# Kernel optimization log

Hardware: AMD Instinct MI355X
Metric: run time of the kernel (lower is better)

The kernel has to match this reference:

```python
import jax, jax.numpy as jnp
import numpy as np
from jax import lax

B, S, N, DIM = 4, 512, 16, 8
D_MODEL, D_STATE = 1024, 64
INPUT_SIZE = N * DIM
LN_EPS = 1e-5


def setup_inputs() -> dict:
    key = jax.random.key(0)
    ks = jax.random.split(key, 8)
    s = 0.02
    x = jax.random.normal(ks[0], (B, S, N, DIM), dtype=jnp.float32)
    W_emb = jax.random.normal(ks[1], (INPUT_SIZE, D_MODEL), dtype=jnp.float32) * s
    b_emb = jnp.zeros((D_MODEL,), jnp.float32)
    W_xp = jax.random.normal(ks[2], (D_MODEL, 2 * D_STATE + 1), dtype=jnp.float32) * s
    b_xp = jnp.zeros((2 * D_STATE + 1,), jnp.float32)
    # A init: -exp(arange(1, d_state+1) * 0.1), matching the torch module
    A = -jnp.exp(jnp.arange(1, D_STATE + 1, dtype=jnp.float32) * 0.1)
    Dp = jnp.ones((D_MODEL,), jnp.float32)
    gamma = jnp.ones((D_MODEL,), jnp.float32)
    beta = jnp.zeros((D_MODEL,), jnp.float32)
    W_out = jax.random.normal(ks[3], (D_MODEL, INPUT_SIZE), dtype=jnp.float32) * s
    b_out = jnp.zeros((INPUT_SIZE,), jnp.float32)
    return {"x": x, "W_emb": W_emb, "b_emb": b_emb, "W_xp": W_xp, "b_xp": b_xp,
            "A": A, "Dp": Dp, "gamma": gamma, "beta": beta,
            "W_out": W_out, "b_out": b_out}


def reference(x, W_emb, b_emb, W_xp, b_xp, A, Dp, gamma, beta, W_out, b_out):
    b, s, n, dim = x.shape
    d_state = A.shape[0]
    d_model = W_emb.shape[1]
    u = x.reshape(b, s, n * dim) @ W_emb + b_emb            # [B,S,dm]
    sel = u @ W_xp + b_xp                                    # [B,S,2*ds+1]
    delta = jax.nn.softplus(sel[..., 0:1]) * 0.01            # [B,S,1]
    Bs = sel[..., 1:1 + d_state]                             # [B,S,ds]
    Cs = sel[..., 1 + d_state:]                              # [B,S,ds]
    A_bar = jnp.exp(delta * A)                               # [B,S,ds]
    B_bar = delta * Bs                                       # [B,S,ds]

    def step(h, inp):
        a_t, b_t, c_t, u_t = inp                             # [B,ds],[B,ds],[B,ds],[B,dm]
        h = h * a_t[:, None, :] + b_t[:, None, :] * u_t[:, :, None]  # [B,dm,ds]
        y_t = jnp.einsum('bmd,bd->bm', h, c_t) + u_t * Dp
        return h, y_t

    h0 = jnp.zeros((b, d_model, d_state), x.dtype)
    xs = (jnp.swapaxes(A_bar, 0, 1), jnp.swapaxes(B_bar, 0, 1),
          jnp.swapaxes(Cs, 0, 1), jnp.swapaxes(u, 0, 1))
    _, ys = lax.scan(step, h0, xs)                           # ys: [S,B,dm]
    y = jnp.swapaxes(ys, 0, 1)                               # [B,S,dm]
    mu = y.mean(-1, keepdims=True)
    var = y.var(-1, keepdims=True)
    yn = (y - mu) / jnp.sqrt(var + LN_EPS) * gamma + beta
    pred = yn @ W_out + b_out                                # [B,S,N*D]
    return pred.reshape(b, s, n, dim)
```

## Files before the change

### kernel.cpp

```cpp
#include <hip/hip_runtime.h>
#include <cstddef>

typedef __attribute__((ext_vector_type(8))) short short8;
typedef __attribute__((ext_vector_type(4))) float f32x4;

constexpr int ROWS = 2048;
constexpr int CL   = 32;

__device__ inline ushort tobf(float f) {
  union { float f; unsigned u; } v; v.f = f;
  return (ushort)((v.u + 0x7FFFu + ((v.u >> 16) & 1u)) >> 16);
}

__global__ __launch_bounds__(256)
void prep(const float* __restrict__ Wemb, const float* __restrict__ Wxp,
          const float* __restrict__ Wout, const float* __restrict__ x,
          ushort* __restrict__ WembT, ushort* __restrict__ wBCdT,
          ushort* __restrict__ WoutT, ushort* __restrict__ xbf) {
  int idx = blockIdx.x * 256 + threadIdx.x;
  if (idx < 131072) {
    int n = idx >> 7, k = idx & 127;
    WembT[idx] = tobf(Wemb[k * 1024 + n]);
  } else if (idx < 327680) {
    int j = idx - 131072;
    int n = j >> 10, k = j & 1023;
    float v = (n < 128) ? Wxp[k * 129 + 1 + n] : (n == 128 ? Wxp[k * 129] : 0.f);
    wBCdT[j] = tobf(v);
  } else if (idx < 458752) {
    int j = idx - 327680;
    int n = j >> 10, k = j & 1023;
    WoutT[j] = tobf(Wout[k * 128 + n]);
  } else if (idx < 720896) {
    int j = idx - 458752;
    xbf[j] = tobf(x[j]);
  }
}

template<bool SPLIT>
__global__ __launch_bounds__(256)
void gemm_bt_bf16(const ushort* __restrict__ A, const ushort* __restrict__ BT,
                  const float* __restrict__ bias, float* __restrict__ C,
                  ushort* __restrict__ Cbf, int M, int N, int K) {
  __shared__ __align__(16) ushort sA[8192];
  __shared__ __align__(16) ushort sB[8192];
  const int t  = threadIdx.x;
  const int n0 = blockIdx.x * 64;
  const int m0 = blockIdx.y * 64;
  const int kc = blockIdx.z << 7;

  #pragma unroll
  for (int i = 0; i < 4; ++i) {
    int c = t + (i << 8);
    int row = c >> 4, kk = (c & 15) << 3;
    float4 va = *(const float4*)(A  + (size_t)(m0 + row) * K + kc + kk);
    float4 vb = *(const float4*)(BT + (size_t)(n0 + row) * K + kc + kk);
    int byteoff = ((row << 8) + (kk << 1)) ^ ((row & 7) << 4);
    *(float4*)((char*)sA + byteoff) = va;
    *(float4*)((char*)sB + byteoff) = vb;
  }
  __syncthreads();

  const int lane = t & 63, w = t >> 6;
  const int wr = w << 4;
  const int colsel = lane & 15;
  const int kg = lane >> 4;

  short8 a[4];
  {
    int arow = wr + colsel;
    int lin = (arow << 8) + (kg << 4);
    int swz = (arow & 7) << 4;
    #pragma unroll
    for (int ks = 0; ks < 4; ++ks)
      a[ks] = *(const short8*)((const char*)sA + ((lin + (ks << 6)) ^ swz));
  }

  f32x4 acc[4];
  #pragma unroll
  for (int nf = 0; nf < 4; ++nf) acc[nf] = (f32x4)(0.f);

  #pragma unroll
  for (int nf = 0; nf < 4; ++nf) {
    int brow = (nf << 4) + colsel;
    int lin = (brow << 8) + (kg << 4);
    int swz = (brow & 7) << 4;
    #pragma unroll
    for (int ks = 0; ks < 4; ++ks) {
      short8 b = *(const short8*)((const char*)sB + ((lin + (ks << 6)) ^ swz));
      acc[nf] = __builtin_amdgcn_mfma_f32_16x16x32_bf16(a[ks], b, acc[nf], 0, 0, 0);
    }
  }

  const int r4 = kg << 2;
  float* Cp = C;
  if (SPLIT) Cp += (size_t)blockIdx.z * (size_t)M * N;
  #pragma unroll
  for (int nf = 0; nf < 4; ++nf) {
    int gn = n0 + (nf << 4) + colsel;
    #pragma unroll
    for (int reg = 0; reg < 4; ++reg) {
      int gm = m0 + wr + r4 + reg;
      if (SPLIT) {
        Cp[(size_t)gm * N + gn] = acc[nf][reg];
      } else {
        float v = acc[nf][reg] + bias[gn];
        C[(size_t)gm * N + gn] = v;
        Cbf[(size_t)gm * N + gn] = tobf(v);
      }
    }
  }
}

__global__ __launch_bounds__(256)
void k2e_epilogue(const float* __restrict__ part, const float* __restrict__ bxp,
                  const float* __restrict__ A, float* __restrict__ abc) {
  int gid = blockIdx.x * 256 + threadIdx.x;
  int row = gid >> 6, d = gid & 63;
  const size_t PN = (size_t)ROWS * 192;
  float sb = 0.f, sc = 0.f, dr = 0.f;
  #pragma unroll
  for (int z = 0; z < 8; ++z) {
    const float* p = part + z * PN + (size_t)row * 192;
    sb += p[d];
    sc += p[64 + d];
    dr += p[128];
  }
  sb += bxp[1 + d];
  sc += bxp[65 + d];
  float xv = dr + bxp[0];
  float sp = (xv > 15.f) ? xv : log1pf(__expf(xv));
  float delta = 0.01f * sp;
  float* o = abc + (size_t)row * 192;
  o[d]       = __expf(delta * A[d]);
  o[64 + d]  = delta * sb;
  o[128 + d] = sc;
}

__global__ __launch_bounds__(256)
void scan_sum(const float* __restrict__ u, const float* __restrict__ abc,
              float* __restrict__ cst, float* __restrict__ Ach) {
  __shared__ __align__(16) float sbuf[CL * 192];
  const int t = threadIdx.x, lane = t & 63, w = t >> 6;
  const int tc = blockIdx.x % 15;
  const int mg = (blockIdx.x / 15) & 3;
  const int b  = blockIdx.x / 60;
  const int r0 = b * 512 + tc * CL;

  const float4* src = (const float4*)(abc + (size_t)r0 * 192);
  #pragma unroll
  for (int i = 0; i < 6; ++i)
    ((float4*)sbuf)[t + i * 256] = src[t + i * 256];
  __syncthreads();

  const int m = (mg * 4 + w) * 64 + lane;
  const float* ub = u + (size_t)r0 * 1024 + m;
  const bool doAp = (mg == 0 && w == 0);

  float2 h[32];
  float2 ap[32];
  #pragma unroll
  for (int j = 0; j < 32; ++j) { h[j] = make_float2(0.f, 0.f); ap[j] = make_float2(1.f, 1.f); }

  float u0 = ub[0];
  float u1 = ub[1024];
  for (int s = 0; s < CL; ++s) {
    int sn = (s < CL - 3) ? s + 2 : CL - 1;
    float u2 = ub[(size_t)sn * 1024];
    const float* L = sbuf + s * 192;
    #pragma unroll
    for (int jj = 0; jj < 16; ++jj) {
      float4 a4 = *(const float4*)&L[4 * jj];
      float4 b4 = *(const float4*)&L[64 + 4 * jj];
      h[2 * jj].x     = fmaf(h[2 * jj].x,     a4.x, b4.x * u0);
      h[2 * jj].y     = fmaf(h[2 * jj].y,     a4.y, b4.y * u0);
      h[2 * jj + 1].x = fmaf(h[2 * jj + 1].x, a4.z, b4.z * u0);
      h[2 * jj + 1].y = fmaf(h[2 * jj + 1].y, a4.w, b4.w * u0);
    }
    if (doAp) {
      #pragma unroll
      for (int jj = 0; jj < 16; ++jj) {
        float4 a4 = *(const float4*)&L[4 * jj];
        ap[2 * jj].x     *= a4.x;
        ap[2 * jj].y     *= a4.y;
        ap[2 * jj + 1].x *= a4.z;
        ap[2 * jj + 1].y *= a4.w;
      }
    }
    u0 = u1; u1 = u2;
  }

  size_t cbase = (((size_t)b * 15 + tc) * 64) * 1024 + m;
  #pragma unroll
  for (int j = 0; j < 32; ++j) {
    cst[cbase + (size_t)(2 * j)     * 1024] = h[j].x;
    cst[cbase + (size_t)(2 * j + 1) * 1024] = h[j].y;
  }
  if (doAp && lane == 0) {
    float2* ad = (float2*)&Ach[((size_t)b * 15 + tc) * 64];
    #pragma unroll
    for (int j = 0; j < 32; ++j) ad[j] = ap[j];
  }
}

__global__ __launch_bounds__(256)
void scan_comb(float* __restrict__ cst, const float* __restrict__ Ach) {
  int g = blockIdx.x * 256 + threadIdx.x;
  int b = g >> 16;
  int rem = g & 65535;
  int d = rem >> 10;
  int m = rem & 1023;
  float h = 0.f;
  for (int t2 = 0; t2 < 15; ++t2) {
    size_t idx = (((size_t)(b * 15 + t2)) * 64 + d) * 1024 + m;
    h = fmaf(Ach[(b * 15 + t2) * 64 + d], h, cst[idx]);
    cst[idx] = h;
  }
}

__global__ __launch_bounds__(256)
void scan_out(const float* __restrict__ u, const float* __restrict__ abc,
              const float* __restrict__ cst, const float* __restrict__ Dp,
              float* __restrict__ y) {
  __shared__ __align__(16) float sbuf[CL * 192];
  const int t = threadIdx.x, lane = t & 63, w = t >> 6;
  const int tc = blockIdx.x & 15;
  const int mg = (blockIdx.x >> 4) & 3;
  const int b  = blockIdx.x >> 6;
  const int r0 = b * 512 + tc * CL;

  const float4* src = (const float4*)(abc + (size_t)r0 * 192);
  #pragma unroll
  for (int i = 0; i < 6; ++i)
    ((float4*)sbuf)[t + i * 256] = src[t + i * 256];
  __syncthreads();

  const int m = (mg * 4 + w) * 64 + lane;
  const float* ub = u + (size_t)r0 * 1024 + m;
  float*       yb = y + (size_t)r0 * 1024 + m;
  const float dp = Dp[m];

  float2 h[32];
  if (tc == 0) {
    #pragma unroll
    for (int j = 0; j < 32; ++j) h[j] = make_float2(0.f, 0.f);
  } else {
    size_t cbase = (((size_t)b * 15 + (tc - 1)) * 64) * 1024 + m;
    #pragma unroll
    for (int j = 0; j < 32; ++j) {
      h[j].x = cst[cbase + (size_t)(2 * j)     * 1024];
      h[j].y = cst[cbase + (size_t)(2 * j + 1) * 1024];
    }
  }

  float u0 = ub[0];
  float u1 = ub[1024];
  for (int s = 0; s < CL; ++s) {
    int sn = (s < CL - 3) ? s + 2 : CL - 1;
    float u2 = ub[(size_t)sn * 1024];
    const float* L = sbuf + s * 192;
    float y0 = 0.f, y1 = 0.f, y2 = 0.f, y3 = 0.f;
    #pragma unroll
    for (int jj = 0; jj < 16; ++jj) {
      float4 a4 = *(const float4*)&L[4 * jj];
      float4 b4 = *(const float4*)&L[64 + 4 * jj];
      float4 c4 = *(const float4*)&L[128 + 4 * jj];
      h[2 * jj].x     = fmaf(h[2 * jj].x,     a4.x, b4.x * u0);
      h[2 * jj].y     = fmaf(h[2 * jj].y,     a4.y, b4.y * u0);
      h[2 * jj + 1].x = fmaf(h[2 * jj + 1].x, a4.z, b4.z * u0);
      h[2 * jj + 1].y = fmaf(h[2 * jj + 1].y, a4.w, b4.w * u0);
      y0 = fmaf(c4.x, h[2 * jj].x,     y0);
      y1 = fmaf(c4.y, h[2 * jj].y,     y1);
      y2 = fmaf(c4.z, h[2 * jj + 1].x, y2);
      y3 = fmaf(c4.w, h[2 * jj + 1].y, y3);
    }
    yb[(size_t)s * 1024] = (y0 + y1) + (y2 + y3) + u0 * dp;
    u0 = u1; u1 = u2;
  }
}

__global__ __launch_bounds__(256)
void k4a_ln(const float* __restrict__ y, const float* __restrict__ gamma,
            const float* __restrict__ beta, ushort* __restrict__ ynbf) {
  __shared__ float red[8];
  int t = threadIdx.x, lane = t & 63, wv = t >> 6;
  int row = blockIdx.x;
  float4 v = *(const float4*)&y[(size_t)row * 1024 + t * 4];
  float s1 = v.x + v.y + v.z + v.w;
  float s2 = v.x * v.x + v.y * v.y + v.z * v.z + v.w * v.w;
  #pragma unroll
  for (int o = 32; o; o >>= 1) {
    s1 += __shfl_xor(s1, o, 64);
    s2 += __shfl_xor(s2, o, 64);
  }
  if (lane == 0) { red[wv] = s1; red[4 + wv] = s2; }
  __syncthreads();
  float S1 = red[0] + red[1] + red[2] + red[3];
  float S2 = red[4] + red[5] + red[6] + red[7];
  float mean = S1 * (1.f / 1024.f);
  float var  = S2 * (1.f / 1024.f) - mean * mean;
  float rstd = rsqrtf(var + 1e-5f);
  float4 g  = *(const float4*)&gamma[t * 4];
  float4 be = *(const float4*)&beta[t * 4];
  ushort4 o;
  o.x = tobf((v.x - mean) * rstd * g.x + be.x);
  o.y = tobf((v.y - mean) * rstd * g.y + be.y);
  o.z = tobf((v.z - mean) * rstd * g.z + be.z);
  o.w = tobf((v.w - mean) * rstd * g.w + be.w);
  *(ushort4*)&ynbf[(size_t)row * 1024 + t * 4] = o;
}

__global__ __launch_bounds__(256)
void k4c_out(const float* __restrict__ part, const float* __restrict__ bout,
             float* __restrict__ out) {
  int g4 = blockIdx.x * 256 + threadIdx.x;
  size_t idx = (size_t)g4 * 4;
  const size_t PN = (size_t)ROWS * 128;
  float4 s = *(const float4*)&part[idx];
  #pragma unroll
  for (int z = 1; z < 8; ++z) {
    float4 p = *(const float4*)&part[z * PN + idx];
    s.x += p.x; s.y += p.y; s.z += p.z; s.w += p.w;
  }
  float4 bb = *(const float4*)&bout[idx & 127];
  s.x += bb.x; s.y += bb.y; s.z += bb.z; s.w += bb.w;
  *(float4*)&out[idx] = s;
}

extern "C" void kernel_launch(void* const* d_in, const int* in_sizes, int n_in,
                              void* d_out, int out_size, void* d_ws, size_t ws_size,
                              hipStream_t stream) {
  const float* x     = (const float*)d_in[0];
  const float* W_emb = (const float*)d_in[1];
  const float* b_emb = (const float*)d_in[2];
  const float* W_xp  = (const float*)d_in[3];
  const float* b_xp  = (const float*)d_in[4];
  const float* A     = (const float*)d_in[5];
  const float* Dp    = (const float*)d_in[6];
  const float* gamma = (const float*)d_in[7];
  const float* beta  = (const float*)d_in[8];
  const float* W_out = (const float*)d_in[9];
  const float* b_out = (const float*)d_in[10];
  float* out = (float*)d_out;
  float* ws  = (float*)d_ws;

  float* u    = ws;
  float* y    = u + 2097152;
  float* abc  = y + 2097152;
  float* part = abc + 393216;
  float* cst  = part + 3145728;
  float* Ach  = cst + 3932160;
  ushort* ubf   = (ushort*)(Ach + 4096);
  ushort* ynbf  = ubf + 2097152;
  ushort* xbf   = ynbf + 2097152;
  ushort* WembT = xbf + 262144;
  ushort* wBCdT = WembT + 131072;
  ushort* WoutT = wBCdT + 196608;

  prep<<<2816, 256, 0, stream>>>(W_emb, W_xp, W_out, x, WembT, wBCdT, WoutT, xbf);
  gemm_bt_bf16<false><<<dim3(16, 32, 1), 256, 0, stream>>>(
      xbf, WembT, b_emb, u, ubf, 2048, 1024, 128);
  gemm_bt_bf16<true><<<dim3(3, 32, 8), 256, 0, stream>>>(
      ubf, wBCdT, nullptr, part, nullptr, 2048, 192, 1024);
  k2e_epilogue<<<512, 256, 0, stream>>>(part, b_xp, A, abc);
  scan_sum<<<240, 256, 0, stream>>>(u, abc, cst, Ach);
  scan_comb<<<1024, 256, 0, stream>>>(cst, Ach);
  scan_out<<<256, 256, 0, stream>>>(u, abc, cst, Dp, y);
  k4a_ln<<<2048, 256, 0, stream>>>(y, gamma, beta, ynbf);
  gemm_bt_bf16<true><<<dim3(2, 32, 8), 256, 0, stream>>>(
      ynbf, WoutT, nullptr, part, nullptr, 2048, 128, 1024);
  k4c_out<<<256, 256, 0, stream>>>(part, b_out, out);
}
```

Baseline: 156.6 us.

## Fuse all stages into one persistent kernel with grid-wide barriers

Replaces the ten-launch pipeline with a single persistent 256-block kernel that runs each stage in sequence, separated by atomic-counter grid barriers. Split-K partial buffers and their reduction kernels are dropped in favour of atomicAdd into pre-initialised outputs, and the scans read the bf16 copy of u instead of an fp32 copy. The aim is to remove launch overhead and the extra partial-sum traffic. In exchange, the spin barriers require all 256 blocks to be co-resident, fewer blocks are available for the larger phases, and atomic accumulation makes the summation order nondeterministic.

```diff
diff --git a/kernel.cpp b/kernel.cpp
--- a/kernel.cpp
+++ b/kernel.cpp
@@ -4,369 +4,371 @@
 typedef __attribute__((ext_vector_type(8))) short short8;
 typedef __attribute__((ext_vector_type(4))) float f32x4;
 
-constexpr int ROWS = 2048;
-constexpr int CL   = 32;
+constexpr int CL = 32;
+constexpr int NB = 256;
 
 __device__ inline ushort tobf(float f) {
   union { float f; unsigned u; } v; v.f = f;
   return (ushort)((v.u + 0x7FFFu + ((v.u >> 16) & 1u)) >> 16);
 }
-
-__global__ __launch_bounds__(256)
-void prep(const float* __restrict__ Wemb, const float* __restrict__ Wxp,
-          const float* __restrict__ Wout, const float* __restrict__ x,
-          ushort* __restrict__ WembT, ushort* __restrict__ wBCdT,
-          ushort* __restrict__ WoutT, ushort* __restrict__ xbf) {
-  int idx = blockIdx.x * 256 + threadIdx.x;
-  if (idx < 131072) {
-    int n = idx >> 7, k = idx & 127;
-    WembT[idx] = tobf(Wemb[k * 1024 + n]);
-  } else if (idx < 327680) {
-    int j = idx - 131072;
-    int n = j >> 10, k = j & 1023;
-    float v = (n < 128) ? Wxp[k * 129 + 1 + n] : (n == 128 ? Wxp[k * 129] : 0.f);
-    wBCdT[j] = tobf(v);
-  } else if (idx < 458752) {
-    int j = idx - 327680;
-    int n = j >> 10, k = j & 1023;
-    WoutT[j] = tobf(Wout[k * 128 + n]);
-  } else if (idx < 720896) {
-    int j = idx - 458752;
-    xbf[j] = tobf(x[j]);
-  }
-}
-
-template<bool SPLIT>
-__global__ __launch_bounds__(256)
-void gemm_bt_bf16(const ushort* __restrict__ A, const ushort* __restrict__ BT,
-                  const float* __restrict__ bias, float* __restrict__ C,
-                  ushort* __restrict__ Cbf, int M, int N, int K) {
-  __shared__ __align__(16) ushort sA[8192];
-  __shared__ __align__(16) ushort sB[8192];
-  const int t  = threadIdx.x;
-  const int n0 = blockIdx.x * 64;
-  const int m0 = blockIdx.y * 64;
-  const int kc = blockIdx.z << 7;
-
-  #pragma unroll
-  for (int i = 0; i < 4; ++i) {
-    int c = t + (i << 8);
-    int row = c >> 4, kk = (c & 15) << 3;
-    float4 va = *(const float4*)(A  + (size_t)(m0 + row) * K + kc + kk);
-    float4 vb = *(const float4*)(BT + (size_t)(n0 + row) * K + kc + kk);
-    int byteoff = ((row << 8) + (kk << 1)) ^ ((row & 7) << 4);
-    *(float4*)((char*)sA + byteoff) = va;
-    *(float4*)((char*)sB + byteoff) = vb;
-  }
+__device__ inline float frombf(ushort u) {
+  union { unsigned u; float f; } v; v.u = ((unsigned)u) << 16; return v.f;
+}
+
+__global__ void bar_init(unsigned* cnt) {
+  if (threadIdx.x < 16) cnt[threadIdx.x] = 0;
+}
+
+__device__ __forceinline__ void gbar(unsigned* cnt, int phase) {
   __syncthreads();
+  if (threadIdx.x == 0) {
+    __threadfence();
+    atomicAdd(&cnt[phase], 1u);
+    while (__hip_atomic_load(&cnt[phase], __ATOMIC_RELAXED,
+                             __HIP_MEMORY_SCOPE_AGENT) < (unsigned)NB)
+      __builtin_amdgcn_s_sleep(2);
+    __threadfence();
+  }
+  __syncthreads();
+}
+
+template<int MODE>
+__device__ __forceinline__ void gemm_phase(
+    int vb, int nxt, int kchunk,
+    const ushort* __restrict__ Ab, const ushort* __restrict__ BT,
+    const float* __restrict__ bias, float* __restrict__ Cf,
+    ushort* __restrict__ Cbf, int M, int N, int K, char* SMEM) {
+  ushort* sA = (ushort*)SMEM;
+  ushort* sB = (ushort*)(SMEM + 16384);
+  const int t = threadIdx.x;
+  const int bx = vb % nxt;
+  const int rest = vb / nxt;
+  const int by = rest & 31;
+  const int bz = rest >> 5;
+  const int n0 = bx * 64, m0 = by * 64;
+  const int k0 = (MODE == 1) ? bz * kchunk : 0;
+  const int k1 = (MODE == 1) ? k0 + kchunk : K;
 
   const int lane = t & 63, w = t >> 6;
   const int wr = w << 4;
   const int colsel = lane & 15;
   const int kg = lane >> 4;
 
-  short8 a[4];
-  {
-    int arow = wr + colsel;
-    int lin = (arow << 8) + (kg << 4);
-    int swz = (arow & 7) << 4;
-    #pragma unroll
-    for (int ks = 0; ks < 4; ++ks)
-      a[ks] = *(const short8*)((const char*)sA + ((lin + (ks << 6)) ^ swz));
-  }
-
   f32x4 acc[4];
   #pragma unroll
   for (int nf = 0; nf < 4; ++nf) acc[nf] = (f32x4)(0.f);
 
-  #pragma unroll
-  for (int nf = 0; nf < 4; ++nf) {
-    int brow = (nf << 4) + colsel;
-    int lin = (brow << 8) + (kg << 4);
-    int swz = (brow & 7) << 4;
-    #pragma unroll
-    for (int ks = 0; ks < 4; ++ks) {
-      short8 b = *(const short8*)((const char*)sB + ((lin + (ks << 6)) ^ swz));
-      acc[nf] = __builtin_amdgcn_mfma_f32_16x16x32_bf16(a[ks], b, acc[nf], 0, 0, 0);
-    }
-  }
-
+  for (int kc = k0; kc < k1; kc += 128) {
+    __syncthreads();
+    #pragma unroll
+    for (int i = 0; i < 4; ++i) {
+      int c = t + (i << 8);
+      int row = c >> 4, kk = (c & 15) << 3;
+      float4 va  = *(const float4*)(Ab + (size_t)(m0 + row) * K + kc + kk);
+      float4 vb4 = *(const float4*)(BT + (size_t)(n0 + row) * K + kc + kk);
+      int byteoff = ((row << 8) + (kk << 1)) ^ ((row & 7) << 4);
+      *(float4*)((char*)sA + byteoff) = va;
+      *(float4*)((char*)sB + byteoff) = vb4;
+    }
+    __syncthreads();
+    short8 a[4];
+    {
+      int arow = wr + colsel;
+      int lin = (arow << 8) + (kg << 4);
+      int swz = (arow & 7) << 4;
+      #pragma unroll
+      for (int ks = 0; ks < 4; ++ks)
+        a[ks] = *(const short8*)((const char*)sA + ((lin + (ks << 6)) ^ swz));
+    }
+    #pragma unroll
+    for (int nf = 0; nf < 4; ++nf) {
+      int brow = (nf << 4) + colsel;
+      int lin = (brow << 8) + (kg << 4);
+      int swz = (brow & 7) << 4;
+      #pragma unroll
+      for (int ks = 0; ks < 4; ++ks) {
+        short8 b = *(const short8*)((const char*)sB + ((lin + (ks << 6)) ^ swz));
+        acc[nf] = __builtin_amdgcn_mfma_f32_16x16x32_bf16(a[ks], b, acc[nf], 0, 0, 0);
+      }
+    }
+  }
   const int r4 = kg << 2;
-  float* Cp = C;
-  if (SPLIT) Cp += (size_t)blockIdx.z * (size_t)M * N;
   #pragma unroll
   for (int nf = 0; nf < 4; ++nf) {
     int gn = n0 + (nf << 4) + colsel;
     #pragma unroll
     for (int reg = 0; reg < 4; ++reg) {
       int gm = m0 + wr + r4 + reg;
-      if (SPLIT) {
-        Cp[(size_t)gm * N + gn] = acc[nf][reg];
+      if (MODE == 0) {
+        Cbf[(size_t)gm * N + gn] = tobf(acc[nf][reg] + bias[gn]);
       } else {
-        float v = acc[nf][reg] + bias[gn];
-        C[(size_t)gm * N + gn] = v;
-        Cbf[(size_t)gm * N + gn] = tobf(v);
-      }
-    }
-  }
-}
-
-__global__ __launch_bounds__(256)
-void k2e_epilogue(const float* __restrict__ part, const float* __restrict__ bxp,
-                  const float* __restrict__ A, float* __restrict__ abc) {
-  int gid = blockIdx.x * 256 + threadIdx.x;
-  int row = gid >> 6, d = gid & 63;
-  const size_t PN = (size_t)ROWS * 192;
-  float sb = 0.f, sc = 0.f, dr = 0.f;
-  #pragma unroll
-  for (int z = 0; z < 8; ++z) {
-    const float* p = part + z * PN + (size_t)row * 192;
-    sb += p[d];
-    sc += p[64 + d];
-    dr += p[128];
-  }
-  sb += bxp[1 + d];
-  sc += bxp[65 + d];
-  float xv = dr + bxp[0];
-  float sp = (xv > 15.f) ? xv : log1pf(__expf(xv));
-  float delta = 0.01f * sp;
-  float* o = abc + (size_t)row * 192;
-  o[d]       = __expf(delta * A[d]);
-  o[64 + d]  = delta * sb;
-  o[128 + d] = sc;
-}
-
-__global__ __launch_bounds__(256)
-void scan_sum(const float* __restrict__ u, const float* __restrict__ abc,
-              float* __restrict__ cst, float* __restrict__ Ach) {
-  __shared__ __align__(16) float sbuf[CL * 192];
+        atomicAdd(&Cf[(size_t)gm * N + gn], acc[nf][reg]);
+      }
+    }
+  }
+}
+
+__global__ __launch_bounds__(256) void mamba_mega(
+    const float* __restrict__ x, const float* __restrict__ Wemb,
+    const float* __restrict__ bemb, const float* __restrict__ Wxp,
+    const float* __restrict__ bxp, const float* __restrict__ A,
+    const float* __restrict__ Dp, const float* __restrict__ gamma,
+    const float* __restrict__ beta, const float* __restrict__ Wout,
+    const float* __restrict__ bout, float* __restrict__ out,
+    float* __restrict__ ws) {
+  const int bid = blockIdx.x;
   const int t = threadIdx.x, lane = t & 63, w = t >> 6;
-  const int tc = blockIdx.x % 15;
-  const int mg = (blockIdx.x / 15) & 3;
-  const int b  = blockIdx.x / 60;
-  const int r0 = b * 512 + tc * CL;
-
-  const float4* src = (const float4*)(abc + (size_t)r0 * 192);
-  #pragma unroll
-  for (int i = 0; i < 6; ++i)
-    ((float4*)sbuf)[t + i * 256] = src[t + i * 256];
-  __syncthreads();
-
-  const int m = (mg * 4 + w) * 64 + lane;
-  const float* ub = u + (size_t)r0 * 1024 + m;
-  const bool doAp = (mg == 0 && w == 0);
-
-  float2 h[32];
-  float2 ap[32];
-  #pragma unroll
-  for (int j = 0; j < 32; ++j) { h[j] = make_float2(0.f, 0.f); ap[j] = make_float2(1.f, 1.f); }
-
-  float u0 = ub[0];
-  float u1 = ub[1024];
-  for (int s = 0; s < CL; ++s) {
-    int sn = (s < CL - 3) ? s + 2 : CL - 1;
-    float u2 = ub[(size_t)sn * 1024];
-    const float* L = sbuf + s * 192;
-    #pragma unroll
-    for (int jj = 0; jj < 16; ++jj) {
-      float4 a4 = *(const float4*)&L[4 * jj];
-      float4 b4 = *(const float4*)&L[64 + 4 * jj];
-      h[2 * jj].x     = fmaf(h[2 * jj].x,     a4.x, b4.x * u0);
-      h[2 * jj].y     = fmaf(h[2 * jj].y,     a4.y, b4.y * u0);
-      h[2 * jj + 1].x = fmaf(h[2 * jj + 1].x, a4.z, b4.z * u0);
-      h[2 * jj + 1].y = fmaf(h[2 * jj + 1].y, a4.w, b4.w * u0);
-    }
-    if (doAp) {
-      #pragma unroll
-      for (int jj = 0; jj < 16; ++jj) {
-        float4 a4 = *(const float4*)&L[4 * jj];
-        ap[2 * jj].x     *= a4.x;
-        ap[2 * jj].y     *= a4.y;
-        ap[2 * jj + 1].x *= a4.z;
-        ap[2 * jj + 1].y *= a4.w;
-      }
-    }
-    u0 = u1; u1 = u2;
-  }
-
-  size_t cbase = (((size_t)b * 15 + tc) * 64) * 1024 + m;
-  #pragma unroll
-  for (int j = 0; j < 32; ++j) {
-    cst[cbase + (size_t)(2 * j)     * 1024] = h[j].x;
-    cst[cbase + (size_t)(2 * j + 1) * 1024] = h[j].y;
-  }
-  if (doAp && lane == 0) {
-    float2* ad = (float2*)&Ach[((size_t)b * 15 + tc) * 64];
-    #pragma unroll
-    for (int j = 0; j < 32; ++j) ad[j] = ap[j];
-  }
-}
-
-__global__ __launch_bounds__(256)
-void scan_comb(float* __restrict__ cst, const float* __restrict__ Ach) {
-  int g = blockIdx.x * 256 + threadIdx.x;
-  int b = g >> 16;
-  int rem = g & 65535;
-  int d = rem >> 10;
-  int m = rem & 1023;
-  float h = 0.f;
-  for (int t2 = 0; t2 < 15; ++t2) {
-    size_t idx = (((size_t)(b * 15 + t2)) * 64 + d) * 1024 + m;
-    h = fmaf(Ach[(b * 15 + t2) * 64 + d], h, cst[idx]);
-    cst[idx] = h;
-  }
-}
-
-__global__ __launch_bounds__(256)
-void scan_out(const float* __restrict__ u, const float* __restrict__ abc,
-              const float* __restrict__ cst, const float* __restrict__ Dp,
-              float* __restrict__ y) {
-  __shared__ __align__(16) float sbuf[CL * 192];
-  const int t = threadIdx.x, lane = t & 63, w = t >> 6;
-  const int tc = blockIdx.x & 15;
-  const int mg = (blockIdx.x >> 4) & 3;
-  const int b  = blockIdx.x >> 6;
-  const int r0 = b * 512 + tc * CL;
-
-  const float4* src = (const float4*)(abc + (size_t)r0 * 192);
-  #pragma unroll
-  for (int i = 0; i < 6; ++i)
-    ((float4*)sbuf)[t + i * 256] = src[t + i * 256];
-  __syncthreads();
-
-  const int m = (mg * 4 + w) * 64 + lane;
-  const float* ub = u + (size_t)r0 * 1024 + m;
-  float*       yb = y + (size_t)r0 * 1024 + m;
-  const float dp = Dp[m];
-
-  float2 h[32];
-  if (tc == 0) {
-    #pragma unroll
-    for (int j = 0; j < 32; ++j) h[j] = make_float2(0.f, 0.f);
-  } else {
-    size_t cbase = (((size_t)b * 15 + (tc - 1)) * 64) * 1024 + m;
-    #pragma unroll
-    for (int j = 0; j < 32; ++j) {
-      h[j].x = cst[cbase + (size_t)(2 * j)     * 1024];
-      h[j].y = cst[cbase + (size_t)(2 * j + 1) * 1024];
-    }
-  }
-
-  float u0 = ub[0];
-  float u1 = ub[1024];
-  for (int s = 0; s < CL; ++s) {
-    int sn = (s < CL - 3) ? s + 2 : CL - 1;
-    float u2 = ub[(size_t)sn * 1024];
-    const float* L = sbuf + s * 192;
-    float y0 = 0.f, y1 = 0.f, y2 = 0.f, y3 = 0.f;
-    #pragma unroll
-    for (int jj = 0; jj < 16; ++jj) {
-      float4 a4 = *(const float4*)&L[4 * jj];
-      float4 b4 = *(const float4*)&L[64 + 4 * jj];
-      float4 c4 = *(const float4*)&L[128 + 4 * jj];
-      h[2 * jj].x     = fmaf(h[2 * jj].x,     a4.x, b4.x * u0);
-      h[2 * jj].y     = fmaf(h[2 * jj].y,     a4.y, b4.y * u0);
-      h[2 * jj + 1].x = fmaf(h[2 * jj + 1].x, a4.z, b4.z * u0);
-      h[2 * jj + 1].y = fmaf(h[2 * jj + 1].y, a4.w, b4.w * u0);
-      y0 = fmaf(c4.x, h[2 * jj].x,     y0);
-      y1 = fmaf(c4.y, h[2 * jj].y,     y1);
-      y2 = fmaf(c4.z, h[2 * jj + 1].x, y2);
-      y3 = fmaf(c4.w, h[2 * jj + 1].y, y3);
-    }
-    yb[(size_t)s * 1024] = (y0 + y1) + (y2 + y3) + u0 * dp;
-    u0 = u1; u1 = u2;
-  }
-}
-
-__global__ __launch_bounds__(256)
-void k4a_ln(const float* __restrict__ y, const float* __restrict__ gamma,
-            const float* __restrict__ beta, ushort* __restrict__ ynbf) {
-  __shared__ float red[8];
-  int t = threadIdx.x, lane = t & 63, wv = t >> 6;
-  int row = blockIdx.x;
-  float4 v = *(const float4*)&y[(size_t)row * 1024 + t * 4];
-  float s1 = v.x + v.y + v.z + v.w;
-  float s2 = v.x * v.x + v.y * v.y + v.z * v.z + v.w * v.w;
-  #pragma unroll
-  for (int o = 32; o; o >>= 1) {
-    s1 += __shfl_xor(s1, o, 64);
-    s2 += __shfl_xor(s2, o, 64);
-  }
-  if (lane == 0) { red[wv] = s1; red[4 + wv] = s2; }
-  __syncthreads();
-  float S1 = red[0] + red[1] + red[2] + red[3];
-  float S2 = red[4] + red[5] + red[6] + red[7];
-  float mean = S1 * (1.f / 1024.f);
-  float var  = S2 * (1.f / 1024.f) - mean * mean;
-  float rstd = rsqrtf(var + 1e-5f);
-  float4 g  = *(const float4*)&gamma[t * 4];
-  float4 be = *(const float4*)&beta[t * 4];
-  ushort4 o;
-  o.x = tobf((v.x - mean) * rstd * g.x + be.x);
-  o.y = tobf((v.y - mean) * rstd * g.y + be.y);
-  o.z = tobf((v.z - mean) * rstd * g.z + be.z);
-  o.w = tobf((v.w - mean) * rstd * g.w + be.w);
-  *(ushort4*)&ynbf[(size_t)row * 1024 + t * 4] = o;
-}
-
-__global__ __launch_bounds__(256)
-void k4c_out(const float* __restrict__ part, const float* __restrict__ bout,
-             float* __restrict__ out) {
-  int g4 = blockIdx.x * 256 + threadIdx.x;
-  size_t idx = (size_t)g4 * 4;
-  const size_t PN = (size_t)ROWS * 128;
-  float4 s = *(const float4*)&part[idx];
-  #pragma unroll
-  for (int z = 1; z < 8; ++z) {
-    float4 p = *(const float4*)&part[z * PN + idx];
-    s.x += p.x; s.y += p.y; s.z += p.z; s.w += p.w;
-  }
-  float4 bb = *(const float4*)&bout[idx & 127];
-  s.x += bb.x; s.y += bb.y; s.z += bb.z; s.w += bb.w;
-  *(float4*)&out[idx] = s;
-}
-
-extern "C" void kernel_launch(void* const* d_in, const int* in_sizes, int n_in,
-                              void* d_out, int out_size, void* d_ws, size_t ws_size,
-                              hipStream_t stream) {
-  const float* x     = (const float*)d_in[0];
-  const float* W_emb = (const float*)d_in[1];
-  const float* b_emb = (const float*)d_in[2];
-  const float* W_xp  = (const float*)d_in[3];
-  const float* b_xp  = (const float*)d_in[4];
-  const float* A     = (const float*)d_in[5];
-  const float* Dp    = (const float*)d_in[6];
-  const float* gamma = (const float*)d_in[7];
-  const float* beta  = (const float*)d_in[8];
-  const float* W_out = (const float*)d_in[9];
-  const float* b_out = (const float*)d_in[10];
-  float* out = (float*)d_out;
-  float* ws  = (float*)d_ws;
-
-  float* u    = ws;
-  float* y    = u + 2097152;
-  float* abc  = y + 2097152;
-  float* part = abc + 393216;
-  float* cst  = part + 3145728;
-  float* Ach  = cst + 3932160;
-  ushort* ubf   = (ushort*)(Ach + 4096);
+  __shared__ __align__(16) char SMEM[32768];
+
+  float* sel = ws;
+  float* abc = ws + 393216;
+  float* cst = ws + 786432;
+  float* y   = ws + 4718592;
+  float* Ach = ws + 6815744;
+  unsigned* cnt = (unsigned*)(ws + 6819840);
+  ushort* ubf   = (ushort*)(ws + 6819856);
   ushort* ynbf  = ubf + 2097152;
   ushort* xbf   = ynbf + 2097152;
   ushort* WembT = xbf + 262144;
   ushort* wBCdT = WembT + 131072;
   ushort* WoutT = wBCdT + 196608;
 
-  prep<<<2816, 256, 0, stream>>>(W_emb, W_xp, W_out, x, WembT, wBCdT, WoutT, xbf);
-  gemm_bt_bf16<false><<<dim3(16, 32, 1), 256, 0, stream>>>(
-      xbf, WembT, b_emb, u, ubf, 2048, 1024, 128);
-  gemm_bt_bf16<true><<<dim3(3, 32, 8), 256, 0, stream>>>(
-      ubf, wBCdT, nullptr, part, nullptr, 2048, 192, 1024);
-  k2e_epilogue<<<512, 256, 0, stream>>>(part, b_xp, A, abc);
-  scan_sum<<<240, 256, 0, stream>>>(u, abc, cst, Ach);
-  scan_comb<<<1024, 256, 0, stream>>>(cst, Ach);
-  scan_out<<<256, 256, 0, stream>>>(u, abc, cst, Dp, y);
-  k4a_ln<<<2048, 256, 0, stream>>>(y, gamma, beta, ynbf);
-  gemm_bt_bf16<true><<<dim3(2, 32, 8), 256, 0, stream>>>(
-      ynbf, WoutT, nullptr, part, nullptr, 2048, 128, 1024);
-  k4c_out<<<256, 256, 0, stream>>>(part, b_out, out);
-}
+  for (int vb = bid; vb < 2816; vb += NB) {
+    int idx = vb * 256 + t;
+    if (idx < 131072) {
+      int k = idx >> 10, n = idx & 1023;
+      WembT[n * 128 + k] = tobf(Wemb[idx]);
+    } else if (idx < 263168) {
+      int j = idx - 131072;
+      int k = j / 129, c = j - k * 129;
+      ushort v2 = tobf(Wxp[j]);
+      if (c == 0) wBCdT[128 * 1024 + k] = v2;
+      else        wBCdT[(c - 1) * 1024 + k] = v2;
+    } else if (idx < 327680) {
+      int j = idx - 263168;
+      wBCdT[129 * 1024 + j] = 0;
+    } else if (idx < 458752) {
+      int j = idx - 327680;
+      WoutT[(j & 127) * 1024 + (j >> 7)] = tobf(Wout[j]);
+    } else if (idx < 720896) {
+      int j = idx - 458752;
+      xbf[j] = tobf(x[j]);
+    }
+  }
+  gbar(cnt, 0);
+
+  for (int i = bid * 256 + t; i < 393216; i += NB * 256) {
+    int c = i % 192;
+    sel[i] = (c < 128) ? bxp[1 + c] : (c == 128 ? bxp[0] : 0.f);
+  }
+  for (int vb = bid; vb < 512; vb += NB)
+    gemm_phase<0>(vb, 16, 0, xbf, WembT, bemb, nullptr, ubf,
+                  2048, 1024, 128, SMEM);
+  gbar(cnt, 1);
+
+  for (int vb = bid; vb < 384; vb += NB)
+    gemm_phase<1>(vb, 3, 256, ubf, wBCdT, nullptr, sel, nullptr,
+                  2048, 192, 1024, SMEM);
+  gbar(cnt, 2);
+
+  for (int vb = bid; vb < 512; vb += NB) {
+    int gid = vb * 256 + t;
+    int row = gid >> 6, d = gid & 63;
+    const float* s = sel + (size_t)row * 192;
+    float sb = s[d], sc = s[64 + d], xv = s[128];
+    float sp = (xv > 15.f) ? xv : log1pf(__expf(xv));
+    float delta = 0.01f * sp;
+    float* o = abc + (size_t)row * 192;
+    o[d]       = __expf(delta * A[d]);
+    o[64 + d]  = delta * sb;
+    o[128 + d] = sc;
+  }
+  gbar(cnt, 3);
+
+  for (int vb = bid; vb < 240; vb += NB) {
+    float* sbuf = (float*)SMEM;
+    const int tc = vb % 15;
+    const int mg = (vb / 15) & 3;
+    const int b = vb / 60;
+    const int r0 = b * 512 + tc * CL;
+    __syncthreads();
+    const float4* src = (const float4*)(abc + (size_t)r0 * 192);
+    #pragma unroll
+    for (int i = 0; i < 6; ++i)
+      ((float4*)sbuf)[t + i * 256] = src[t + i * 256];
+    __syncthreads();
+    const int m = (mg * 4 + w) * 64 + lane;
+    const ushort* ub = ubf + (size_t)r0 * 1024 + m;
+    const bool doAp = (mg == 0 && w == 0);
+    float2 h[32], ap[32];
+    #pragma unroll
+    for (int j = 0; j < 32; ++j) { h[j] = make_float2(0.f, 0.f); ap[j] = make_float2(1.f, 1.f); }
+    float u0 = frombf(ub[0]);
+    float u1 = frombf(ub[1024]);
+    for (int s = 0; s < CL; ++s) {
+      int sn = (s < CL - 3) ? s + 2 : CL - 1;
+      float u2 = frombf(ub[(size_t)sn * 1024]);
+      const float* L = sbuf + s * 192;
+      #pragma unroll
+      for (int jj = 0; jj < 16; ++jj) {
+        float4 a4 = *(const float4*)&L[4 * jj];
+        float4 b4 = *(const float4*)&L[64 + 4 * jj];
+        h[2 * jj].x     = fmaf(h[2 * jj].x,     a4.x, b4.x * u0);
+        h[2 * jj].y     = fmaf(h[2 * jj].y,     a4.y, b4.y * u0);
+        h[2 * jj + 1].x = fmaf(h[2 * jj + 1].x, a4.z, b4.z * u0);
+        h[2 * jj + 1].y = fmaf(h[2 * jj + 1].y, a4.w, b4.w * u0);
+      }
+      if (doAp) {
+        #pragma unroll
+        for (int jj = 0; jj < 16; ++jj) {
+          float4 a4 = *(const float4*)&L[4 * jj];
+          ap[2 * jj].x     *= a4.x;
+          ap[2 * jj].y     *= a4.y;
+          ap[2 * jj + 1].x *= a4.z;
+          ap[2 * jj + 1].y *= a4.w;
+        }
+      }
+      u0 = u1; u1 = u2;
+    }
+    size_t cbase = (((size_t)b * 15 + tc) * 64) * 1024 + m;
+    #pragma unroll
+    for (int j = 0; j < 32; ++j) {
+      cst[cbase + (size_t)(2 * j)     * 1024] = h[j].x;
+      cst[cbase + (size_t)(2 * j + 1) * 1024] = h[j].y;
+    }
+    if (doAp && lane == 0) {
+      float2* ad = (float2*)&Ach[((size_t)b * 15 + tc) * 64];
+      #pragma unroll
+      for (int j = 0; j < 32; ++j) ad[j] = ap[j];
+    }
+  }
+  gbar(cnt, 4);
+
+  for (int vb = bid; vb < 1024; vb += NB) {
+    int g = vb * 256 + t;
+    int b = g >> 16;
+    int rem = g & 65535;
+    int d = rem >> 10;
+    int m = rem & 1023;
+    float h = 0.f;
+    for (int t2 = 0; t2 < 15; ++t2) {
+      size_t idx = (((size_t)(b * 15 + t2)) * 64 + d) * 1024 + m;
+      h = fmaf(Ach[(b * 15 + t2) * 64 + d], h, cst[idx]);
+      cst[idx] = h;
+    }
+  }
+  gbar(cnt, 5);
+
+  for (int vb = bid; vb < 256; vb += NB) {
+    float* sbuf = (float*)SMEM;
+    const int tc = vb & 15;
+    const int mg = (vb >> 4) & 3;
+    const int b = vb >> 6;
+    const int r0 = b * 512 + tc * CL;
+    __syncthreads();
+    const float4* src = (const float4*)(abc + (size_t)r0 * 192);
+    #pragma unroll
+    for (int i = 0; i < 6; ++i)
+      ((float4*)sbuf)[t + i * 256] = src[t + i * 256];
+    __syncthreads();
+    const int m = (mg * 4 + w) * 64 + lane;
+    const ushort* ub = ubf + (size_t)r0 * 1024 + m;
+    float* yb = y + (size_t)r0 * 1024 + m;
+    const float dp = Dp[m];
+    float2 h[32];
+    if (tc == 0) {
+      #pragma unroll
+      for (int j = 0; j < 32; ++j) h[j] = make_float2(0.f, 0.f);
+    } else {
+      size_t cbase = (((size_t)b * 15 + (tc - 1)) * 64) * 1024 + m;
+      #pragma unroll
+      for (int j = 0; j < 32; ++j) {
+        h[j].x = cst[cbase + (size_t)(2 * j)     * 1024];
+        h[j].y = cst[cbase + (size_t)(2 * j + 1) * 1024];
+      }
+    }
+    float u0 = frombf(ub[0]);
+    float u1 = frombf(ub[1024]);
+    for (int s = 0; s < CL; ++s) {
+      int sn = (s < CL - 3) ? s + 2 : CL - 1;
+      float u2 = frombf(ub[(size_t)sn * 1024]);
+      const float* L = sbuf + s * 192;
+      float y0 = 0.f, y1 = 0.f, y2 = 0.f, y3 = 0.f;
+      #pragma unroll
+      for (int jj = 0; jj < 16; ++jj) {
+        float4 a4 = *(const float4*)&L[4 * jj];
+        float4 b4 = *(const float4*)&L[64 + 4 * jj];
+        float4 c4 = *(const float4*)&L[128 + 4 * jj];
+        h[2 * jj].x     = fmaf(h[2 * jj].x,     a4.x, b4.x * u0);
+        h[2 * jj].y     = fmaf(h[2 * jj].y,     a4.y, b4.y * u0);
+        h[2 * jj + 1].x = fmaf(h[2 * jj + 1].x, a4.z, b4.z * u0);
+        h[2 * jj + 1].y = fmaf(h[2 * jj + 1].y, a4.w, b4.w * u0);
+        y0 = fmaf(c4.x, h[2 * jj].x,     y0);
+        y1 = fmaf(c4.y, h[2 * jj].y,     y1);
+        y2 = fmaf(c4.z, h[2 * jj + 1].x, y2);
+        y3 = fmaf(c4.w, h[2 * jj + 1].y, y3);
+      }
+      yb[(size_t)s * 1024] = (y0 + y1) + (y2 + y3) + u0 * dp;
+      u0 = u1; u1 = u2;
+    }
+  }
+  gbar(cnt, 6);
+
+  for (int i = bid * 256 + t; i < 262144; i += NB * 256)
+    out[i] = bout[i & 127];
+  for (int vb = bid; vb < 2048; vb += NB) {
+    float* red = (float*)SMEM;
+    int row = vb;
+    float4 v = *(const float4*)&y[(size_t)row * 1024 + t * 4];
+    float s1 = v.x + v.y + v.z + v.w;
+    float s2 = v.x * v.x + v.y * v.y + v.z * v.z + v.w * v.w;
+    #pragma unroll
+    for (int o = 32; o; o >>= 1) {
+      s1 += __shfl_xor(s1, o, 64);
+      s2 += __shfl_xor(s2, o, 64);
+    }
+    __syncthreads();
+    if (lane == 0) { red[w] = s1; red[4 + w] = s2; }
+    __syncthreads();
+    float S1 = red[0] + red[1] + red[2] + red[3];
+    float S2 = red[4] + red[5] + red[6] + red[7];
+    float mean = S1 * (1.f / 1024.f);
+    float var  = S2 * (1.f / 1024.f) - mean * mean;
+    float rstd = rsqrtf(var + 1e-5f);
+    float4 g  = *(const float4*)&gamma[t * 4];
+    float4 be = *(const float4*)&beta[t * 4];
+    ushort4 o4;
+    o4.x = tobf((v.x - mean) * rstd * g.x + be.x);
+    o4.y = tobf((v.y - mean) * rstd * g.y + be.y);
+    o4.z = tobf((v.z - mean) * rstd * g.z + be.z);
+    o4.w = tobf((v.w - mean) * rstd * g.w + be.w);
+    *(ushort4*)&ynbf[(size_t)row * 1024 + t * 4] = o4;
+  }
+  gbar(cnt, 7);
+
+  for (int vb = bid; vb < 256; vb += NB)
+    gemm_phase<1>(vb, 2, 256, ynbf, WoutT, nullptr, out, nullptr,
+                  2048, 128, 1024, SMEM);
+}
+
+extern "C" void kernel_launch(void* const* d_in, const int* in_sizes, int n_in,
+                              void* d_out, int out_size, void* d_ws, size_t ws_size,
+                              hipStream_t stream) {
+  const float* x     = (const float*)d_in[0];
+  const float* Wemb  = (const float*)d_in[1];
+  const float* bemb  = (const float*)d_in[2];
+  const float* Wxp   = (const float*)d_in[3];
+  const float* bxp   = (const float*)d_in[4];
+  const float* A     = (const float*)d_in[5];
+  const float* Dp    = (const float*)d_in[6];
+  const float* gamma = (const float*)d_in[7];
+  const float* beta  = (const float*)d_in[8];
+  const float* Wout  = (const float*)d_in[9];
+  const float* bout  = (const float*)d_in[10];
+  float* out = (float*)d_out;
+  float* ws  = (float*)d_ws;
+
+  bar_init<<<1, 64, 0, stream>>>((unsigned*)(ws + 6819840));
+  mamba_mega<<<NB, 256, 0, stream>>>(x, Wemb, bemb, Wxp, bxp, A, Dp,
+                                     gamma, beta, Wout, bout, out, ws);
+}
```

Measured after the change: 350.4 us. 2.24x slower.
